# Kernel tuning notes

Hardware: AMD Instinct MI355X
Metric: run time of the kernel (lower is better)

The kernel has to match this reference:

```python
import jax, jax.numpy as jnp
import numpy as np

N = 50000        # nodes
E = 800000       # edges (before self-loops)
F_IN = 128       # num_features
G = 500          # graphs in batch
H1, C1 = 4, 32   # conv1 heads / channels per head
C2 = 8           # num_classes (conv2, heads=1, concat=False)
EPS = 1e-5       # BatchNorm eps
SLOPE = 0.2      # LeakyReLU negative slope (PyG GATConv default)


def setup_inputs() -> dict:
    key = jax.random.key(0)
    ks = jax.random.split(key, 12)
    glorot = lambda k, shape, fan: (jax.random.normal(k, shape, jnp.float32) / np.sqrt(fan)).astype(jnp.float32)
    return {
        "x": jax.random.normal(ks[0], (N, F_IN), jnp.float32),
        "bn_gamma": jnp.ones((F_IN,), jnp.float32),
        "bn_beta": jnp.zeros((F_IN,), jnp.float32),
        "W1": glorot(ks[1], (F_IN, H1 * C1), F_IN),
        "att_src1": glorot(ks[2], (H1, C1), C1),
        "att_dst1": glorot(ks[3], (H1, C1), C1),
        "b1": jnp.zeros((H1 * C1,), jnp.float32),
        "W2": glorot(ks[4], (H1 * C1, C2), H1 * C1),
        "att_src2": glorot(ks[5], (1, C2), C2),
        "att_dst2": glorot(ks[6], (1, C2), C2),
        "b2": jnp.zeros((C2,), jnp.float32),
        "edge_index": jax.random.randint(ks[7], (2, E), 0, N),
        "batch": jnp.sort(jax.random.randint(ks[8], (N,), 0, G)),
    }


def _gat(h, src, dst, a_src, a_dst, num_nodes):
    # h: [N,H,C]; src/dst: [Etot] (self-loops included so every dst occurs)
    al = (h * a_src).sum(-1)                 # [N,H] a_src . W x_i
    ar = (h * a_dst).sum(-1)                 # [N,H]
    e = al[src] + ar[dst]                    # [Etot,H]
    e = jnp.where(e > 0, e, SLOPE * e)       # LeakyReLU
    m = jax.lax.stop_gradient(jax.ops.segment_max(e, dst, num_segments=num_nodes))
    ex = jnp.exp(e - m[dst])
    denom = jax.ops.segment_sum(ex, dst, num_segments=num_nodes)
    alpha = ex / (denom[dst] + 1e-16)        # segment softmax over incoming edges
    return jax.ops.segment_sum(h[src] * alpha[..., None], dst, num_segments=num_nodes)


def reference(x, bn_gamma, bn_beta, W1, att_src1, att_dst1, b1, W2, att_src2, att_dst2, b2, edge_index, batch):
    n = x.shape[0]
    loop = jnp.arange(n)
    src = jnp.concatenate([edge_index[0], loop])   # PyG GATConv adds self-loops
    dst = jnp.concatenate([edge_index[1], loop])

    # BatchNorm (batch statistics)
    mean = x.mean(0)
    var = x.var(0)
    x = (x - mean) * jax.lax.rsqrt(var + EPS) * bn_gamma + bn_beta

    # GATConv 1: 4 heads, concat -> [N,128]
    h1 = (x @ W1).reshape(n, H1, C1)
    o1 = _gat(h1, src, dst, att_src1, att_dst1, n).reshape(n, H1 * C1) + b1
    x1 = jax.nn.elu(o1)   # dropout skipped (eval)

    # GATConv 2: 1 head, concat=False -> [N,num_classes]
    h2 = (x1 @ W2).reshape(n, 1, C2)
    o2 = _gat(h2, src, dst, att_src2, att_dst2, n).reshape(n, C2) + b2

    # global mean pool per graph
    cnt = jax.ops.segment_sum(jnp.ones((n,), o2.dtype), batch, num_segments=G)
    pooled = jax.ops.segment_sum(o2, batch, num_segments=G) / jnp.maximum(cnt, 1.0)[:, None]
    return jax.nn.log_softmax(pooled, axis=-1)
```

## Files before the change

### kernel.cpp

```cpp
#include <hip/hip_runtime.h>
#include <hip/hip_fp16.h>
#include <math.h>

#define F1 128
#define C2N 8
#define SLOPE 0.2f
#define EPSBN 1e-5f
#define BCAP 4096
#define SB 4096
#define BSH 7
#define MAXB 1024

typedef float floatx2 __attribute__((ext_vector_type(2)));

__device__ __forceinline__ unsigned fenc(float f){
  unsigned u = __float_as_uint(f);
  return (u & 0x80000000u) ? ~u : (u | 0x80000000u);
}
__device__ __forceinline__ float fdec(unsigned u){
  return (u & 0x80000000u) ? __uint_as_float(u & 0x7FFFFFFFu) : __uint_as_float(~u);
}
__device__ __forceinline__ float2 h2f2(unsigned u){
  __half2 h = *(__half2*)&u;
  return __half22float2(h);
}

__global__ __launch_bounds__(256) void k_bn_deg(const float* __restrict__ x,
    float* __restrict__ sum, float* __restrict__ sumsq, int n,
    const int* __restrict__ ei, int* __restrict__ deg, int E){
  if ((int)blockIdx.x >= 256){
    int e = ((int)blockIdx.x - 256)*256 + threadIdx.x;
    if (e < E) atomicAdd(&deg[ei[E + e]], 1);
    return;
  }
  int t  = threadIdx.x;
  int c4 = (t & 31) * 4;
  int rg = t >> 5;
  float4 s = {0,0,0,0}, q = {0,0,0,0};
  for (int r = blockIdx.x*8 + rg; r < n; r += 2048){
    float4 v = *(const float4*)&x[(size_t)r*F1 + c4];
    s.x += v.x; s.y += v.y; s.z += v.z; s.w += v.w;
    q.x += v.x*v.x; q.y += v.y*v.y; q.z += v.z*v.z; q.w += v.w*v.w;
  }
  s.x += __shfl_xor(s.x, 32); s.y += __shfl_xor(s.y, 32);
  s.z += __shfl_xor(s.z, 32); s.w += __shfl_xor(s.w, 32);
  q.x += __shfl_xor(q.x, 32); q.y += __shfl_xor(q.y, 32);
  q.z += __shfl_xor(q.z, 32); q.w += __shfl_xor(q.w, 32);
  __shared__ float red[2][4][F1];
  int w = t >> 6;
  int l = t & 63;
  if (l < 32){
    *(float4*)&red[0][w][l*4] = s;
    *(float4*)&red[1][w][l*4] = q;
  }
  __syncthreads();
  if (t < 128){
    float a = red[0][0][t] + red[0][1][t] + red[0][2][t] + red[0][3][t];
    atomicAdd(&sum[t], a);
  } else {
    int f = t - 128;
    float a = red[1][0][f] + red[1][1][f] + red[1][2][f] + red[1][3][f];
    atomicAdd(&sumsq[f], a);
  }
}

__global__ __launch_bounds__(256) void k_scan_a_bn(const int* __restrict__ deg,
    int* __restrict__ rowptr, int* __restrict__ bsum, int n,
    const float* __restrict__ sum, const float* __restrict__ sumsq,
    const float* __restrict__ gamma, const float* __restrict__ beta,
    float* __restrict__ ab){
  int nbS = gridDim.x - 1;
  if ((int)blockIdx.x == nbS){
    int f = threadIdx.x;
    if (f < 128){
      float inv_n = 1.f / (float)n;
      float mean = sum[f] * inv_n;
      float var  = sumsq[f] * inv_n - mean*mean;
      float inv  = rsqrtf(var + EPSBN);
      float a = inv * gamma[f];
      ab[f]      = a;
      ab[F1 + f] = beta[f] - mean*a;
    }
    return;
  }
  int t = threadIdx.x;
  int base = blockIdx.x*1024 + t*4;
  int4 v = {0,0,0,0};
  if (base + 3 < n){
    v = *(const int4*)&deg[base];
    v.x += 1; v.y += 1; v.z += 1; v.w += 1;
  } else {
    if (base   < n) v.x = deg[base]   + 1;
    if (base+1 < n) v.y = deg[base+1] + 1;
    if (base+2 < n) v.z = deg[base+2] + 1;
    if (base+3 < n) v.w = deg[base+3] + 1;
  }
  int s = v.x + v.y + v.z + v.w;
  __shared__ int ls[256];
  ls[t] = s; __syncthreads();
  for (int off = 1; off < 256; off <<= 1){
    int u = (t >= off) ? ls[t-off] : 0;
    __syncthreads();
    ls[t] += u;
    __syncthreads();
  }
  int ex = ls[t] - s;
  if (t == 255) bsum[blockIdx.x] = ls[255];
  int4 w;
  w.x = ex;
  w.y = ex + v.x;
  w.z = w.y + v.y;
  w.w = w.z + v.z;
  if (base + 3 < n) *(int4*)&rowptr[base] = w;
  else {
    if (base   < n) rowptr[base]   = w.x;
    if (base+1 < n) rowptr[base+1] = w.y;
    if (base+2 < n) rowptr[base+2] = w.z;
    if (base+3 < n) rowptr[base+3] = w.w;
  }
}

__global__ __launch_bounds__(256) void k_scan_c(int* __restrict__ rowptr,
    int* __restrict__ cursor, const int* __restrict__ bsum, int n){
  int t = threadIdx.x;
  __shared__ int s_boff;
  if (t < 64){
    int b = blockIdx.x;
    int val = 0;
    for (int i = t; i < b; i += 64) val += bsum[i];
    #pragma unroll
    for (int m = 1; m < 64; m <<= 1) val += __shfl_xor(val, m);
    if (t == 0) s_boff = val;
  }
  __syncthreads();
  int boff = s_boff;
  if (t == 0 && blockIdx.x == gridDim.x - 1)
    rowptr[n] = boff + bsum[blockIdx.x];
  int base = blockIdx.x*1024 + t*4;
  if (base + 3 < n){
    int4 v = *(int4*)&rowptr[base];
    v.x += boff; v.y += boff; v.z += boff; v.w += boff;
    *(int4*)&rowptr[base] = v;
    *(int4*)&cursor[base] = v;
  } else {
    for (int k = 0; k < 4; ++k)
      if (base + k < n){
        int v = rowptr[base+k] + boff;
        rowptr[base+k] = v; cursor[base+k] = v;
      }
  }
}

__global__ __launch_bounds__(256) void k_gemm1_binit(const float* __restrict__ x,
    const float* __restrict__ ab, const float* __restrict__ W1,
    const float* __restrict__ asrc, const float* __restrict__ adst,
    unsigned char* __restrict__ h1, float* __restrict__ al, float* __restrict__ ar,
    int n, const int* __restrict__ rowptr, int* __restrict__ bcur, int NB, int nbG){
  if ((int)blockIdx.x >= nbG){
    int b = ((int)blockIdx.x - nbG)*256 + threadIdx.x;
    if (b < NB) bcur[b*16] = rowptr[b<<BSH];
    return;
  }
  const int j    = threadIdx.x & 127;
  const int half = threadIdx.x >> 7;
  const int r0   = blockIdx.x * 16 + half*8;
  __shared__ float xs[16][F1];
  float A = ab[j], B = ab[F1 + j];
  int nr = n - r0; if (nr > 8) nr = 8; if (nr < 0) nr = 0;
  for (int rr = 0; rr < nr; ++rr)
    xs[half*8+rr][j] = x[(size_t)(r0+rr)*F1 + j] * A + B;
  __syncthreads();
  float acc[8] = {0,0,0,0,0,0,0,0};
  for (int k = 0; k < F1; ++k){
    float w = W1[k*F1 + j];
    #pragma unroll
    for (int rr = 0; rr < 8; ++rr) acc[rr] += xs[half*8+rr][k] * w;
  }
  float as = asrc[j], ad = adst[j];
  for (int rr = 0; rr < nr; ++rr){
    float hv = acc[rr];
    int pk = __builtin_amdgcn_cvt_pk_fp8_f32(hv, hv, 0, false);
    h1[(size_t)(r0+rr)*F1 + j] = (unsigned char)(pk & 0xFF);
    float vs = hv*as, vd = hv*ad;
    #pragma unroll
    for (int mk = 1; mk < 32; mk <<= 1){
      vs += __shfl_xor(vs, mk);
      vd += __shfl_xor(vd, mk);
    }
    if ((j & 31) == 0){
      al[(r0+rr)*4 + (j>>5)] = vs;
      ar[(r0+rr)*4 + (j>>5)] = vd;
    }
  }
}

__global__ __launch_bounds__(256) void k_colmax(const float* __restrict__ v,
    unsigned* __restrict__ out, int total, int H){
  int tid = blockIdx.x*256 + threadIdx.x;
  int stride = gridDim.x*256;
  float mx = -1e30f;
  for (int i = tid; i < total; i += stride)
    mx = fmaxf(mx, v[i]);
  for (int m = H; m < 64; m <<= 1)
    mx = fmaxf(mx, __shfl_xor(mx, m));
  int lane = threadIdx.x & 63;
  if (lane < H) atomicMax(&out[lane], fenc(mx));
}

__global__ __launch_bounds__(256) void k_sort_cmax(const int* __restrict__ ei,
    int* __restrict__ bcur, int2* __restrict__ tmp, int E, int Etot, int NB,
    int nbS, const float* __restrict__ al1, unsigned* __restrict__ almax1, int totalC){
  __shared__ int hist[MAXB];
  __shared__ int hbase[MAXB];
  __shared__ int2 stage[SB];
  if ((int)blockIdx.x >= nbS){
    int bid = (int)blockIdx.x - nbS;
    int tid = bid*256 + threadIdx.x;
    int stride = 128*256;
    float mx = -1e30f;
    for (int i = tid; i < totalC; i += stride)
      mx = fmaxf(mx, al1[i]);
    mx = fmaxf(mx, __shfl_xor(mx, 4));
    mx = fmaxf(mx, __shfl_xor(mx, 8));
    mx = fmaxf(mx, __shfl_xor(mx, 16));
    mx = fmaxf(mx, __shfl_xor(mx, 32));
    int lane = threadIdx.x & 63;
    if (lane < 4) atomicMax(&almax1[lane], fenc(mx));
    return;
  }
  int base_e = blockIdx.x * SB;
  int cnt = Etot - base_e; if (cnt > SB) cnt = SB;
  for (int i = threadIdx.x; i < NB; i += 256) hist[i] = 0;
  __syncthreads();
  for (int i = threadIdx.x; i < cnt; i += 256){
    int e = base_e + i;
    int s = (e < E) ? ei[e]     : (e - E);
    int d = (e < E) ? ei[E + e] : (e - E);
    stage[i] = make_int2(s, d);
    atomicAdd(&hist[d>>BSH], 1);
  }
  __syncthreads();
  for (int i = threadIdx.x; i < NB; i += 256){
    int c = hist[i];
    hbase[i] = c ? atomicAdd(&bcur[i*16], c) : 0;
    hist[i] = 0;
  }
  __syncthreads();
  for (int i = threadIdx.x; i < cnt; i += 256){
    int2 sd = stage[i];
    int b = sd.y >> BSH;
    int off = atomicAdd(&hist[b], 1);
    tmp[hbase[b] + off] = sd;
  }
}

__global__ __launch_bounds__(256) void k_fill2(const int* __restrict__ rowptr,
    const int2* __restrict__ tmp, int* __restrict__ csr_src,
    int* __restrict__ csr_dst, int* __restrict__ cursor, int n, int NB){
  int b = blockIdx.x;
  int node0 = b << BSH;
  int node1 = node0 + (1<<BSH); if (node1 > n) node1 = n;
  int base = rowptr[node0];
  int endp = rowptr[node1];
  int size = endp - base;
  __shared__ int lcur[1<<BSH];
  __shared__ int2 lout[BCAP];
  if (size <= BCAP){
    if (threadIdx.x < (1<<BSH)){
      int nd = node0 + threadIdx.x;
      lcur[threadIdx.x] = (nd < node1) ? rowptr[nd] - base : 0;
    }
    __syncthreads();
    for (int i = threadIdx.x; i < size; i += 256){
      int2 sd = tmp[base + i];
      int rel = atomicAdd(&lcur[sd.y & ((1<<BSH)-1)], 1);
      lout[rel] = sd;
    }
    __syncthreads();
    for (int i = threadIdx.x; i < size; i += 256){
      int2 sd = lout[i];
      csr_src[base + i] = sd.x;
      csr_dst[base + i] = sd.y;
    }
  } else {
    for (int i = threadIdx.x; i < size; i += 256){
      int2 sd = tmp[base + i];
      int pos = atomicAdd(&cursor[sd.y], 1);
      csr_src[pos] = sd.x;
      csr_dst[pos] = sd.y;
    }
  }
}

__global__ __launch_bounds__(256) void k_gat1(const int* __restrict__ rowptr,
    const int* __restrict__ csr_src, const float* __restrict__ al,
    const float* __restrict__ ar, const unsigned* __restrict__ almax,
    const unsigned char* __restrict__ h1, const float* __restrict__ b1,
    const float* __restrict__ W2, const float* __restrict__ as2,
    const float* __restrict__ ad2, __half* __restrict__ h2,
    float* __restrict__ al2, float* __restrict__ ar2, int n){
  __shared__ float w2s[1024];
  for (int a = threadIdx.x; a < 1024; a += 256){
    int fs = a & 15;
    int es = (a >> 4) & 3;
    int r  = a >> 6;
    int kk = r >> 1;
    int jj = r & 1;
    w2s[a] = W2[(fs*8 + kk)*C2N + es*2 + jj];
  }
  __syncthreads();
  int node = blockIdx.x*4 + (threadIdx.x >> 6);
  if (node >= n) return;
  int lane = threadIdx.x & 63;
  int es = lane >> 4;
  int fs = lane & 15;
  int h  = fs >> 2;
  int f0 = fs << 3;
  int beg = rowptr[node], end = rowptr[node+1];
  float ard = ar[node*4 + h];
  float ub = fdec(almax[h]) + ard;
  ub = ub > 0.f ? ub : SLOPE*ub;
  float a0=0.f,a1=0.f,a2=0.f,a3=0.f,a4=0.f,a5=0.f,a6=0.f,a7=0.f,den=0.f;
  int c = beg;
  #define EDGE_GRP(SV, ALV, HV) { \
    float v_ = ALV + ard; v_ = v_ > 0.f ? v_ : SLOPE*v_; \
    float w_ = __expf(v_ - ub); \
    den += w_; \
    floatx2 r0_ = __builtin_amdgcn_cvt_pk_f32_fp8(HV.x, false); \
    floatx2 r1_ = __builtin_amdgcn_cvt_pk_f32_fp8(HV.x, true); \
    floatx2 r2_ = __builtin_amdgcn_cvt_pk_f32_fp8(HV.y, false); \
    floatx2 r3_ = __builtin_amdgcn_cvt_pk_f32_fp8(HV.y, true); \
    a0 += w_*r0_.x; a1 += w_*r0_.y; a2 += w_*r1_.x; a3 += w_*r1_.y; \
    a4 += w_*r2_.x; a5 += w_*r2_.y; a6 += w_*r3_.x; a7 += w_*r3_.y; }
  for (; c + 16 <= end; c += 16){
    int sA = csr_src[c + es];
    int sB = csr_src[c + 4 + es];
    int sC = csr_src[c + 8 + es];
    int sD = csr_src[c + 12 + es];
    float alA = al[sA*4 + h];
    float alB = al[sB*4 + h];
    float alC = al[sC*4 + h];
    float alD = al[sD*4 + h];
    uint2 hvA = *(const uint2*)&h1[((size_t)sA<<7) + f0];
    uint2 hvB = *(const uint2*)&h1[((size_t)sB<<7) + f0];
    uint2 hvC = *(const uint2*)&h1[((size_t)sC<<7) + f0];
    uint2 hvD = *(const uint2*)&h1[((size_t)sD<<7) + f0];
    EDGE_GRP(sA, alA, hvA)
    EDGE_GRP(sB, alB, hvB)
    EDGE_GRP(sC, alC, hvC)
    EDGE_GRP(sD, alD, hvD)
  }
  for (; c + 8 <= end; c += 8){
    int sA = csr_src[c + es];
    int sB = csr_src[c + 4 + es];
    float alA = al[sA*4 + h];
    float alB = al[sB*4 + h];
    uint2 hvA = *(const uint2*)&h1[((size_t)sA<<7) + f0];
    uint2 hvB = *(const uint2*)&h1[((size_t)sB<<7) + f0];
    EDGE_GRP(sA, alA, hvA)
    EDGE_GRP(sB, alB, hvB)
  }
  #undef EDGE_GRP
  for (; c < end; c += 4){
    int idx = c + es;
    bool ok = idx < end;
    int s = csr_src[ok ? idx : end-1];
    float alv = al[s*4 + h];
    float v = alv + ard; v = v > 0.f ? v : SLOPE*v;
    float wv = __expf(v - ub);
    wv = ok ? wv : 0.f;
    den += wv;
    uint2 hv = *(const uint2*)&h1[((size_t)s<<7) + f0];
    floatx2 p0 = __builtin_amdgcn_cvt_pk_f32_fp8(hv.x, false);
    floatx2 p1 = __builtin_amdgcn_cvt_pk_f32_fp8(hv.x, true);
    floatx2 p2 = __builtin_amdgcn_cvt_pk_f32_fp8(hv.y, false);
    floatx2 p3 = __builtin_amdgcn_cvt_pk_f32_fp8(hv.y, true);
    a0 += wv*p0.x; a1 += wv*p0.y; a2 += wv*p1.x; a3 += wv*p1.y;
    a4 += wv*p2.x; a5 += wv*p2.y; a6 += wv*p3.x; a7 += wv*p3.y;
  }
  #define RED2(X) { X += __shfl_xor(X,16); X += __shfl_xor(X,32); }
  RED2(a0) RED2(a1) RED2(a2) RED2(a3) RED2(a4) RED2(a5) RED2(a6) RED2(a7) RED2(den)
  float inv = 1.f / (den + 1e-16f);
  float4 bA = *(const float4*)&b1[f0];
  float4 bB = *(const float4*)&b1[f0+4];
  float o0 = a0*inv + bA.x, o1 = a1*inv + bA.y;
  float o2 = a2*inv + bA.z, o3 = a3*inv + bA.w;
  float o4 = a4*inv + bB.x, o5 = a5*inv + bB.y;
  float o6 = a6*inv + bB.z, o7 = a7*inv + bB.w;
  o0 = o0 > 0.f ? o0 : __expf(o0) - 1.f;
  o1 = o1 > 0.f ? o1 : __expf(o1) - 1.f;
  o2 = o2 > 0.f ? o2 : __expf(o2) - 1.f;
  o3 = o3 > 0.f ? o3 : __expf(o3) - 1.f;
  o4 = o4 > 0.f ? o4 : __expf(o4) - 1.f;
  o5 = o5 > 0.f ? o5 : __expf(o5) - 1.f;
  o6 = o6 > 0.f ? o6 : __expf(o6) - 1.f;
  o7 = o7 > 0.f ? o7 : __expf(o7) - 1.f;
  const float* wG = w2s + es*16 + fs;
  float gA = 0.f, gB = 0.f;
  gA += o0*wG[0];   gB += o0*wG[64];
  gA += o1*wG[128]; gB += o1*wG[192];
  gA += o2*wG[256]; gB += o2*wG[320];
  gA += o3*wG[384]; gB += o3*wG[448];
  gA += o4*wG[512]; gB += o4*wG[576];
  gA += o5*wG[640]; gB += o5*wG[704];
  gA += o6*wG[768]; gB += o6*wG[832];
  gA += o7*wG[896]; gB += o7*wG[960];
  #define RED4(X) { X += __shfl_xor(X,1); X += __shfl_xor(X,2); \
                    X += __shfl_xor(X,4); X += __shfl_xor(X,8); }
  RED4(gA) RED4(gB)
  #undef RED4
  float pal = gA*as2[es*2] + gB*as2[es*2+1];
  float par = gA*ad2[es*2] + gB*ad2[es*2+1];
  RED2(pal) RED2(par)
  #undef RED2
  if (fs == 0){
    *(__half2*)&h2[((size_t)node<<3) + es*2] = __floats2half2_rn(gA, gB);
  }
  if (lane == 0){
    al2[node] = pal;
    ar2[node] = par;
  }
}

__global__ __launch_bounds__(256) void k_gat2e(const int* __restrict__ csr_src,
    const int* __restrict__ csr_dst, const float* __restrict__ al,
    const float* __restrict__ ar, const unsigned* __restrict__ almax,
    const __half* __restrict__ h2, float* __restrict__ nacc,
    float* __restrict__ nden, int Etot){
  int e = blockIdx.x*256 + threadIdx.x;
  int lane = threadIdx.x & 63;
  bool ok = e < Etot;
  int s = ok ? csr_src[e] : 0;
  int d = ok ? csr_dst[e] : -1;
  float w = 0.f;
  if (ok){
    float ardv = ar[d];
    float v = al[s] + ardv; v = v > 0.f ? v : SLOPE*v;
    float ub = fdec(almax[0]) + ardv; ub = ub > 0.f ? ub : SLOPE*ub;
    w = __expf(v - ub);
  }
  float2 h01 = {0,0}, h23 = {0,0}, h45 = {0,0}, h67 = {0,0};
  if (ok){
    uint4 hv = *(const uint4*)&h2[((size_t)s<<3)];
    h01 = h2f2(hv.x); h23 = h2f2(hv.y); h45 = h2f2(hv.z); h67 = h2f2(hv.w);
  }
  float a0 = w*h01.x, a1 = w*h01.y, a2 = w*h23.x, a3 = w*h23.y;
  float a4 = w*h45.x, a5 = w*h45.y, a6 = w*h67.x, a7 = w*h67.y;
  float den = w;
  #pragma unroll
  for (int off = 1; off < 64; off <<= 1){
    int du = __shfl_up(d, off);
    bool add = (lane >= off) && (du == d);
    float t;
    t = __shfl_up(a0, off); if (add) a0 += t;
    t = __shfl_up(a1, off); if (add) a1 += t;
    t = __shfl_up(a2, off); if (add) a2 += t;
    t = __shfl_up(a3, off); if (add) a3 += t;
    t = __shfl_up(a4, off); if (add) a4 += t;
    t = __shfl_up(a5, off); if (add) a5 += t;
    t = __shfl_up(a6, off); if (add) a6 += t;
    t = __shfl_up(a7, off); if (add) a7 += t;
    t = __shfl_up(den, off); if (add) den += t;
  }
  int dn = __shfl_down(d, 1);
  bool tail = (lane == 63) || (dn != d);
  if (tail && d >= 0){
    float* np = nacc + ((size_t)d<<3);
    atomicAdd(np+0, a0); atomicAdd(np+1, a1);
    atomicAdd(np+2, a2); atomicAdd(np+3, a3);
    atomicAdd(np+4, a4); atomicAdd(np+5, a5);
    atomicAdd(np+6, a6); atomicAdd(np+7, a7);
    atomicAdd(&nden[d], den);
  }
}

__global__ __launch_bounds__(256) void k_fin2(const float* __restrict__ nacc,
    const float* __restrict__ nden, const float* __restrict__ b2,
    const int* __restrict__ batch, float* __restrict__ pooled,
    float* __restrict__ cnt, int n){
  int t = blockIdx.x*256 + threadIdx.x;
  int node = t >> 3, j = t & 7;
  if (node >= n) return;
  float o = nacc[t] / (nden[node] + 1e-16f) + b2[j];
  int g = batch[node];
  atomicAdd(&pooled[g*C2N + j], o);
  if (j == 0) atomicAdd(&cnt[g], 1.f);
}

__global__ __launch_bounds__(256) void k_final(const float* __restrict__ pooled,
    const float* __restrict__ cnt, float* __restrict__ out, int G){
  int g = blockIdx.x*blockDim.x + threadIdx.x;
  if (g >= G) return;
  float c = cnt[g]; c = c > 1.f ? c : 1.f;
  float p[8]; float mx = -1e30f;
  #pragma unroll
  for (int j = 0; j < 8; ++j){ p[j] = pooled[g*8+j] / c; mx = fmaxf(mx, p[j]); }
  float s = 0.f;
  #pragma unroll
  for (int j = 0; j < 8; ++j) s += expf(p[j]-mx);
  float lse = mx + logf(s);
  #pragma unroll
  for (int j = 0; j < 8; ++j) out[g*8+j] = p[j] - lse;
}

extern "C" void kernel_launch(void* const* d_in, const int* in_sizes, int n_in,
                              void* d_out, int out_size, void* d_ws, size_t ws_size,
                              hipStream_t stream){
  const float* x    = (const float*)d_in[0];
  const float* gam  = (const float*)d_in[1];
  const float* bet  = (const float*)d_in[2];
  const float* W1   = (const float*)d_in[3];
  const float* as1  = (const float*)d_in[4];
  const float* ad1  = (const float*)d_in[5];
  const float* b1   = (const float*)d_in[6];
  const float* W2   = (const float*)d_in[7];
  const float* as2  = (const float*)d_in[8];
  const float* ad2  = (const float*)d_in[9];
  const float* b2   = (const float*)d_in[10];
  const int*   ei   = (const int*)d_in[11];
  const int*   batch= (const int*)d_in[12];

  int N = in_sizes[0] / F1;
  int E = in_sizes[11] / 2;
  int G = out_size / C2N;
  int Etot = E + N;
  int nb = (N + 1023) / 1024;
  int NB = (N + (1<<BSH) - 1) >> BSH;
  int nbG = (N + 15) / 16;
  int nbB = (NB + 255) / 256;
  int nbS = (Etot + SB - 1) / SB;

  char* base = (char*)d_ws;
  auto alloc = [&](size_t bytes)->char*{
    char* p = base; base += (bytes + 15) & ~15ull; return p;
  };

  char* A0 = base;
  float*    sum     = (float*)alloc(128*4);
  float*    sumsq   = (float*)alloc(128*4);
  int*      deg     = (int*)alloc((size_t)N*4);
  float*    pooled  = (float*)alloc((size_t)G*C2N*4);
  float*    cnt     = (float*)alloc((size_t)G*4);
  unsigned* almax1u = (unsigned*)alloc(16);
  unsigned* almax2u = (unsigned*)alloc(16);
  float*    nacc    = (float*)alloc((size_t)N*C2N*4);
  float*    nden    = (float*)alloc((size_t)N*4);
  size_t Abytes = (size_t)(base - A0);
  int*     csr_src = (int*)alloc((size_t)Etot*4);
  int*     csr_dst = (int*)alloc((size_t)Etot*4);
  int2*    tmp     = (int2*)alloc((size_t)Etot*8);
  int*     bcur    = (int*)alloc((size_t)NB*64);
  float*   ab      = (float*)alloc(256*4);
  int*     rowptr  = (int*)alloc(((size_t)N+4)*4);
  int*     cursor  = (int*)alloc((size_t)N*4);
  int*     bsum    = (int*)alloc((size_t)nb*4);
  unsigned char* h1 = (unsigned char*)alloc((size_t)N*F1);
  float*   al1     = (float*)alloc((size_t)N*4*4);
  float*   ar1     = (float*)alloc((size_t)N*4*4);
  __half*  h2      = (__half*)alloc((size_t)N*C2N*2);
  float*   al2     = (float*)alloc((size_t)N*4);
  float*   ar2     = (float*)alloc((size_t)N*4);

  hipMemsetAsync(A0, 0, Abytes, stream);

  k_bn_deg<<<256 + (E + 255)/256, 256, 0, stream>>>(x, sum, sumsq, N, ei, deg, E);
  k_scan_a_bn<<<nb + 1, 256, 0, stream>>>(deg, rowptr, bsum, N, sum, sumsq, gam, bet, ab);
  k_scan_c<<<nb, 256, 0, stream>>>(rowptr, cursor, bsum, N);
  k_gemm1_binit<<<nbG + nbB, 256, 0, stream>>>(x, ab, W1, as1, ad1, h1, al1, ar1, N,
                                               rowptr, bcur, NB, nbG);
  k_sort_cmax<<<nbS + 128, 256, 0, stream>>>(ei, bcur, tmp, E, Etot, NB,
                                             nbS, al1, almax1u, N*4);
  k_fill2<<<NB, 256, 0, stream>>>(rowptr, tmp, csr_src, csr_dst, cursor, N, NB);
  k_gat1<<<(N + 3)/4, 256, 0, stream>>>(rowptr, csr_src, al1, ar1, almax1u, h1, b1,
                                        W2, as2, ad2, h2, al2, ar2, N);
  k_colmax<<<64, 256, 0, stream>>>(al2, almax2u, N, 1);
  k_gat2e<<<(Etot + 255)/256, 256, 0, stream>>>(csr_src, csr_dst, al2, ar2, almax2u, h2, nacc, nden, Etot);
  k_fin2<<<((N*C2N) + 255)/256, 256, 0, stream>>>(nacc, nden, b2, batch, pooled, cnt, N);
  k_final<<<(G + 255)/256, 256, 0, stream>>>(pooled, cnt, (float*)d_out, G);
}
```

Baseline: 261.7 us.

## Fuse scan finalize into GEMM1 launch and final softmax into pooling kernel

The scan-offset kernel is merged into the GEMM1 launch as extra blocks. Bucket cursors are now zero-initialised by the memset and offset by rowptr inside the sort kernel, so the separate bcur init is gone. The final log-softmax is folded into the pooling kernel with a last-block-done atomic counter. Together these remove two kernel launches, at the cost of a threadfence and an atomic counter in every pooling block.

```diff
diff --git a/kernel.cpp b/kernel.cpp
--- a/kernel.cpp
+++ b/kernel.cpp
@@ -120,45 +120,40 @@
   }
 }
 
-__global__ __launch_bounds__(256) void k_scan_c(int* __restrict__ rowptr,
-    int* __restrict__ cursor, const int* __restrict__ bsum, int n){
-  int t = threadIdx.x;
-  __shared__ int s_boff;
-  if (t < 64){
-    int b = blockIdx.x;
-    int val = 0;
-    for (int i = t; i < b; i += 64) val += bsum[i];
-    #pragma unroll
-    for (int m = 1; m < 64; m <<= 1) val += __shfl_xor(val, m);
-    if (t == 0) s_boff = val;
-  }
-  __syncthreads();
-  int boff = s_boff;
-  if (t == 0 && blockIdx.x == gridDim.x - 1)
-    rowptr[n] = boff + bsum[blockIdx.x];
-  int base = blockIdx.x*1024 + t*4;
-  if (base + 3 < n){
-    int4 v = *(int4*)&rowptr[base];
-    v.x += boff; v.y += boff; v.z += boff; v.w += boff;
-    *(int4*)&rowptr[base] = v;
-    *(int4*)&cursor[base] = v;
-  } else {
-    for (int k = 0; k < 4; ++k)
-      if (base + k < n){
-        int v = rowptr[base+k] + boff;
-        rowptr[base+k] = v; cursor[base+k] = v;
-      }
-  }
-}
-
-__global__ __launch_bounds__(256) void k_gemm1_binit(const float* __restrict__ x,
+__global__ __launch_bounds__(256) void k_gemm1_scanc(const float* __restrict__ x,
     const float* __restrict__ ab, const float* __restrict__ W1,
     const float* __restrict__ asrc, const float* __restrict__ adst,
     unsigned char* __restrict__ h1, float* __restrict__ al, float* __restrict__ ar,
-    int n, const int* __restrict__ rowptr, int* __restrict__ bcur, int NB, int nbG){
+    int n, int* __restrict__ rowptr, int* __restrict__ cursor,
+    const int* __restrict__ bsum, int nb, int nbG){
   if ((int)blockIdx.x >= nbG){
-    int b = ((int)blockIdx.x - nbG)*256 + threadIdx.x;
-    if (b < NB) bcur[b*16] = rowptr[b<<BSH];
+    int sb = (int)blockIdx.x - nbG;
+    int t = threadIdx.x;
+    __shared__ int s_boff;
+    if (t < 64){
+      int val = 0;
+      for (int i = t; i < sb; i += 64) val += bsum[i];
+      #pragma unroll
+      for (int m = 1; m < 64; m <<= 1) val += __shfl_xor(val, m);
+      if (t == 0) s_boff = val;
+    }
+    __syncthreads();
+    int boff = s_boff;
+    if (t == 0 && sb == nb - 1)
+      rowptr[n] = boff + bsum[sb];
+    int base = sb*1024 + t*4;
+    if (base + 3 < n){
+      int4 v = *(int4*)&rowptr[base];
+      v.x += boff; v.y += boff; v.z += boff; v.w += boff;
+      *(int4*)&rowptr[base] = v;
+      *(int4*)&cursor[base] = v;
+    } else {
+      for (int k = 0; k < 4; ++k)
+        if (base + k < n){
+          int v = rowptr[base+k] + boff;
+          rowptr[base+k] = v; cursor[base+k] = v;
+        }
+    }
     return;
   }
   const int j    = threadIdx.x & 127;
@@ -208,7 +203,8 @@
 }
 
 __global__ __launch_bounds__(256) void k_sort_cmax(const int* __restrict__ ei,
-    int* __restrict__ bcur, int2* __restrict__ tmp, int E, int Etot, int NB,
+    const int* __restrict__ rowptr, int* __restrict__ bcur,
+    int2* __restrict__ tmp, int E, int Etot, int NB,
     int nbS, const float* __restrict__ al1, unsigned* __restrict__ almax1, int totalC){
   __shared__ int hist[MAXB];
   __shared__ int hbase[MAXB];
@@ -242,7 +238,7 @@
   __syncthreads();
   for (int i = threadIdx.x; i < NB; i += 256){
     int c = hist[i];
-    hbase[i] = c ? atomicAdd(&bcur[i*16], c) : 0;
+    hbase[i] = c ? (rowptr[i<<BSH] + atomicAdd(&bcur[i*16], c)) : 0;
     hist[i] = 0;
   }
   __syncthreads();
@@ -474,33 +470,42 @@
   }
 }
 
-__global__ __launch_bounds__(256) void k_fin2(const float* __restrict__ nacc,
+__global__ __launch_bounds__(256) void k_fin2f(const float* __restrict__ nacc,
     const float* __restrict__ nden, const float* __restrict__ b2,
     const int* __restrict__ batch, float* __restrict__ pooled,
-    float* __restrict__ cnt, int n){
+    float* __restrict__ cnt, float* __restrict__ out, int n, int G,
+    int* __restrict__ done, int nblocks){
   int t = blockIdx.x*256 + threadIdx.x;
   int node = t >> 3, j = t & 7;
-  if (node >= n) return;
-  float o = nacc[t] / (nden[node] + 1e-16f) + b2[j];
-  int g = batch[node];
-  atomicAdd(&pooled[g*C2N + j], o);
-  if (j == 0) atomicAdd(&cnt[g], 1.f);
-}
-
-__global__ __launch_bounds__(256) void k_final(const float* __restrict__ pooled,
-    const float* __restrict__ cnt, float* __restrict__ out, int G){
-  int g = blockIdx.x*blockDim.x + threadIdx.x;
-  if (g >= G) return;
-  float c = cnt[g]; c = c > 1.f ? c : 1.f;
-  float p[8]; float mx = -1e30f;
-  #pragma unroll
-  for (int j = 0; j < 8; ++j){ p[j] = pooled[g*8+j] / c; mx = fmaxf(mx, p[j]); }
-  float s = 0.f;
-  #pragma unroll
-  for (int j = 0; j < 8; ++j) s += expf(p[j]-mx);
-  float lse = mx + logf(s);
-  #pragma unroll
-  for (int j = 0; j < 8; ++j) out[g*8+j] = p[j] - lse;
+  if (node < n){
+    float o = nacc[t] / (nden[node] + 1e-16f) + b2[j];
+    int g = batch[node];
+    atomicAdd(&pooled[g*C2N + j], o);
+    if (j == 0) atomicAdd(&cnt[g], 1.f);
+  }
+  __threadfence();
+  __syncthreads();
+  __shared__ int lastBlock;
+  if (threadIdx.x == 0)
+    lastBlock = (atomicAdd(done, 1) == nblocks - 1);
+  __syncthreads();
+  if (lastBlock){
+    __threadfence();
+    const volatile float* vp = (const volatile float*)pooled;
+    const volatile float* vc = (const volatile float*)cnt;
+    for (int g = threadIdx.x; g < G; g += 256){
+      float c = vc[g]; c = c > 1.f ? c : 1.f;
+      float p[8]; float mx = -1e30f;
+      #pragma unroll
+      for (int jj = 0; jj < 8; ++jj){ p[jj] = vp[g*8+jj] / c; mx = fmaxf(mx, p[jj]); }
+      float s = 0.f;
+      #pragma unroll
+      for (int jj = 0; jj < 8; ++jj) s += expf(p[jj]-mx);
+      float lse = mx + logf(s);
+      #pragma unroll
+      for (int jj = 0; jj < 8; ++jj) out[g*8+jj] = p[jj] - lse;
+    }
+  }
 }
 
 extern "C" void kernel_launch(void* const* d_in, const int* in_sizes, int n_in,
@@ -527,8 +532,8 @@
   int nb = (N + 1023) / 1024;
   int NB = (N + (1<<BSH) - 1) >> BSH;
   int nbG = (N + 15) / 16;
-  int nbB = (NB + 255) / 256;
   int nbS = (Etot + SB - 1) / SB;
+  int nbF = ((N*C2N) + 255) / 256;
 
   char* base = (char*)d_ws;
   auto alloc = [&](size_t bytes)->char*{
@@ -545,11 +550,12 @@
   unsigned* almax2u = (unsigned*)alloc(16);
   float*    nacc    = (float*)alloc((size_t)N*C2N*4);
   float*    nden    = (float*)alloc((size_t)N*4);
+  int*      bcur    = (int*)alloc((size_t)NB*64);
+  int*      done    = (int*)alloc(16);
   size_t Abytes = (size_t)(base - A0);
   int*     csr_src = (int*)alloc((size_t)Etot*4);
   int*     csr_dst = (int*)alloc((size_t)Etot*4);
   int2*    tmp     = (int2*)alloc((size_t)Etot*8);
-  int*     bcur    = (int*)alloc((size_t)NB*64);
   float*   ab      = (float*)alloc(256*4);
   int*     rowptr  = (int*)alloc(((size_t)N+4)*4);
   int*     cursor  = (int*)alloc((size_t)N*4);
@@ -565,16 +571,15 @@
 
   k_bn_deg<<<256 + (E + 255)/256, 256, 0, stream>>>(x, sum, sumsq, N, ei, deg, E);
   k_scan_a_bn<<<nb + 1, 256, 0, stream>>>(deg, rowptr, bsum, N, sum, sumsq, gam, bet, ab);
-  k_scan_c<<<nb, 256, 0, stream>>>(rowptr, cursor, bsum, N);
-  k_gemm1_binit<<<nbG + nbB, 256, 0, stream>>>(x, ab, W1, as1, ad1, h1, al1, ar1, N,
-                                               rowptr, bcur, NB, nbG);
-  k_sort_cmax<<<nbS + 128, 256, 0, stream>>>(ei, bcur, tmp, E, Etot, NB,
+  k_gemm1_scanc<<<nbG + nb, 256, 0, stream>>>(x, ab, W1, as1, ad1, h1, al1, ar1, N,
+                                              rowptr, cursor, bsum, nb, nbG);
+  k_sort_cmax<<<nbS + 128, 256, 0, stream>>>(ei, rowptr, bcur, tmp, E, Etot, NB,
                                              nbS, al1, almax1u, N*4);
   k_fill2<<<NB, 256, 0, stream>>>(rowptr, tmp, csr_src, csr_dst, cursor, N, NB);
   k_gat1<<<(N + 3)/4, 256, 0, stream>>>(rowptr, csr_src, al1, ar1, almax1u, h1, b1,
                                         W2, as2, ad2, h2, al2, ar2, N);
   k_colmax<<<64, 256, 0, stream>>>(al2, almax2u, N, 1);
   k_gat2e<<<(Etot + 255)/256, 256, 0, stream>>>(csr_src, csr_dst, al2, ar2, almax2u, h2, nacc, nden, Etot);
-  k_fin2<<<((N*C2N) + 255)/256, 256, 0, stream>>>(nacc, nden, b2, batch, pooled, cnt, N);
-  k_final<<<(G + 255)/256, 256, 0, stream>>>(pooled, cnt, (float*)d_out, G);
-}
+  k_fin2f<<<nbF, 256, 0, stream>>>(nacc, nden, b2, batch, pooled, cnt,
+                                   (float*)d_out, N, G, done, nbF);
+}
```

After: 328.0 us. 25.4% more time.
